# Kernel tuning notes

Measured on AMD Instinct MI355X. Metric: run time of the kernel, lower is better.

## Reference

```python
import jax, jax.numpy as jnp
import numpy as np

NUM_HEADS = 8
NUM_UNITS = 512


def setup_inputs() -> dict:
    key = jax.random.key(0)
    ks = jax.random.split(key, 5)
    B, S, D = 2, 4096, NUM_UNITS
    scale = 1.0 / np.sqrt(D)
    return {
        "x": jax.random.normal(ks[0], (B, S, D), dtype=jnp.float32),
        "Wq": jax.random.normal(ks[1], (D, NUM_UNITS), dtype=jnp.float32) * scale,
        "Wk": jax.random.normal(ks[2], (D, NUM_UNITS), dtype=jnp.float32) * scale,
        "Wv": jax.random.normal(ks[3], (D, NUM_UNITS), dtype=jnp.float32) * scale,
        "Wo": jax.random.normal(ks[4], (D, NUM_UNITS), dtype=jnp.float32) * scale,
    }


def reference(x, Wq, Wk, Wv, Wo):
    B, S, _ = x.shape
    H = NUM_HEADS
    Dh = NUM_UNITS // H

    # QKV linear projections (self-attention: K_V = (x, x))
    Q = x @ Wq  # [B,S,U]
    K = x @ Wk
    V = x @ Wv

    # split heads -> [B,H,S,Dh]
    def split(t):
        return t.reshape(B, S, H, Dh).transpose(0, 2, 1, 3)

    Qh, Kh, Vh = split(Q), split(K), split(V)

    # scaled dot-product attention, bias = 0, no mask, no dropout (training=False)
    scores = jnp.einsum("bhqd,bhkd->bhqk", Qh, Kh) / jnp.sqrt(
        jnp.asarray(Dh, dtype=x.dtype)
    )
    attn = jax.nn.softmax(scores, axis=-1)
    ctx = jnp.einsum("bhqk,bhkd->bhqd", attn, Vh)

    # combine heads -> [B,S,U], then output projection
    ctx = ctx.transpose(0, 2, 1, 3).reshape(B, S, NUM_UNITS)
    return ctx @ Wo
```

## Files before the change

### kernel.cpp

```cpp
#include <hip/hip_runtime.h>

typedef __attribute__((ext_vector_type(8))) short short8;
typedef __attribute__((ext_vector_type(4))) float f32x4;
typedef __attribute__((ext_vector_type(4))) unsigned short us4;
typedef unsigned short ushort_t;
typedef unsigned int uint_t;

typedef const __attribute__((address_space(1))) void* gas1;
typedef __attribute__((address_space(3))) void* las3;

#define LDS_FENCE()                                            \
  do {                                                         \
    asm volatile("s_waitcnt lgkmcnt(0)" ::: "memory");         \
    __builtin_amdgcn_sched_barrier(0);                         \
  } while (0)

__device__ __forceinline__ ushort_t f2b(float f) {
  union { float f; uint_t u; } v; v.f = f;
  return (ushort_t)((v.u + 0x7fffu + ((v.u >> 16) & 1u)) >> 16);
}

__device__ __forceinline__ float b2f(ushort_t u) {
  union { uint_t u; float f; } v; v.u = ((uint_t)u) << 16;
  return v.f;
}

__device__ __forceinline__ uint_t cvtpk(float lo, float hi) {
  uint_t r;
  asm("v_cvt_pk_bf16_f32 %0, %1, %2" : "=v"(r) : "v"(lo), "v"(hi));
  return r;
}

__device__ __forceinline__ void gld_lds16(const ushort_t* g, void* l) {
  __builtin_amdgcn_global_load_lds((gas1)g, (las3)l, 16, 0, 0);
}

__device__ __forceinline__ float max3f(float a, float b, float c) {
  return fmaxf(fmaxf(a, b), c);
}

__global__ void cvt_x_kernel(const float* __restrict__ x, ushort_t* __restrict__ xb, int n4) {
  int i = blockIdx.x * blockDim.x + threadIdx.x;
  if (i >= n4) return;
  float4 v = ((const float4*)x)[i];
  ushort4 o;
  o.x = f2b(v.x); o.y = f2b(v.y); o.z = f2b(v.z); o.w = f2b(v.w);
  ((ushort4*)xb)[i] = o;
}

__global__ void cvt_wt_kernel(const float* __restrict__ W0, const float* __restrict__ W1,
                              const float* __restrict__ W2, const float* __restrict__ W3,
                              ushort_t* __restrict__ T0, ushort_t* __restrict__ T1,
                              ushort_t* __restrict__ T2, ushort_t* __restrict__ T3) {
  const float* W; ushort_t* T;
  switch (blockIdx.z) {
    case 0: W = W0; T = T0; break;
    case 1: W = W1; T = T1; break;
    case 2: W = W2; T = T2; break;
    default: W = W3; T = T3; break;
  }
  __shared__ ushort_t Tl[64 * 68];
  int t = threadIdx.x;
  int kt = blockIdx.x & 7, nt = blockIdx.x >> 3;
  int krow = t >> 4;
  int ncol = (t & 15) * 4;
#pragma unroll
  for (int j = 0; j < 4; ++j) {
    int k = j * 16 + krow;
    float4 v = *(const float4*)&W[(size_t)(kt * 64 + k) * 512 + nt * 64 + ncol];
    const float* vf = (const float*)&v;
#pragma unroll
    for (int e = 0; e < 4; ++e)
      Tl[(ncol + e) * 68 + k] = f2b(vf[e]);
  }
  __syncthreads();
#pragma unroll
  for (int j = 0; j < 4; ++j) {
    int f = j * 1024 + t * 4;
    int n = f >> 6, k = f & 63;
    *(ushort4*)&T[(size_t)(nt * 64 + n) * 512 + kt * 64 + k] =
        *(const ushort4*)&Tl[n * 68 + k];
  }
}

__global__ __launch_bounds__(256) void gemm_qkv_kernel(
    const ushort_t* __restrict__ A,
    const ushort_t* __restrict__ WqT, const ushort_t* __restrict__ WkT,
    const ushort_t* __restrict__ WvT,
    ushort_t* __restrict__ Qo, ushort_t* __restrict__ Ko, ushort_t* __restrict__ VTo) {
  const int K = 512, N = 512, S = 4096;
  const ushort_t* BT; ushort_t* out; int mode;
  switch (blockIdx.z) {
    case 0: BT = WqT; out = Qo;  mode = 0; break;
    case 1: BT = WkT; out = Ko;  mode = 0; break;
    default: BT = WvT; out = VTo; mode = 1; break;
  }
  __shared__ ushort_t Al[128 * 64];
  __shared__ ushort_t Bl[128 * 64];

  int tid = threadIdx.x, lane = tid & 63, w = tid >> 6;
  int g = lane >> 4, ln = lane & 15;
  int wr = w >> 1, wc = w & 1;
  int m0 = blockIdx.y * 128;
  int n0 = blockIdx.x * 128;

  f32x4 acc[4][4];
  const f32x4 zz = {0.f, 0.f, 0.f, 0.f};
#pragma unroll
  for (int i = 0; i < 4; ++i)
#pragma unroll
    for (int j = 0; j < 4; ++j) acc[i][j] = zz;

  for (int kt = 0; kt < 8; ++kt) {
    __syncthreads();
#pragma unroll
    for (int i = 0; i < 4; ++i) {
      int p = i * 256 + tid, row = p >> 3, sl = p & 7, sp = sl ^ (row & 7);
      gld_lds16(A + (size_t)(m0 + row) * K + kt * 64 + sp * 8,
                (char*)Al + (i * 256 + (tid & 192)) * 16);
    }
#pragma unroll
    for (int i = 0; i < 4; ++i) {
      int p = i * 256 + tid, row = p >> 3, sl = p & 7, sp = sl ^ (row & 7);
      gld_lds16(BT + (size_t)(n0 + row) * K + kt * 64 + sp * 8,
                (char*)Bl + (i * 256 + (tid & 192)) * 16);
    }
    __syncthreads();

#pragma unroll
    for (int kc = 0; kc < 2; ++kc) {
      short8 af[4], bf[4];
#pragma unroll
      for (int mt = 0; mt < 4; ++mt) {
        int row = wr * 64 + mt * 16 + ln;
        af[mt] = *(const short8*)((char*)Al + row * 128 + (((kc * 4 + g) ^ (row & 7)) * 16));
      }
#pragma unroll
      for (int nt = 0; nt < 4; ++nt) {
        int row = wc * 64 + nt * 16 + ln;
        bf[nt] = *(const short8*)((char*)Bl + row * 128 + (((kc * 4 + g) ^ (row & 7)) * 16));
      }
#pragma unroll
      for (int mt = 0; mt < 4; ++mt)
#pragma unroll
        for (int nt = 0; nt < 4; ++nt)
          acc[mt][nt] = __builtin_amdgcn_mfma_f32_16x16x32_bf16(af[mt], bf[nt], acc[mt][nt], 0, 0, 0);
    }
  }

  if (mode == 0) {
#pragma unroll
    for (int mt = 0; mt < 4; ++mt)
#pragma unroll
      for (int nt = 0; nt < 4; ++nt)
#pragma unroll
        for (int jj = 0; jj < 4; ++jj) {
          int m = m0 + wr * 64 + mt * 16 + 4 * g + jj;
          int n = n0 + wc * 64 + nt * 16 + ln;
          out[(size_t)m * N + n] = f2b(acc[mt][nt][jj]);
        }
  } else {
#pragma unroll
    for (int mt = 0; mt < 4; ++mt)
#pragma unroll
      for (int nt = 0; nt < 4; ++nt) {
        int s0 = m0 + wr * 64 + mt * 16 + 4 * g;
        int u = n0 + wc * 64 + nt * 16 + ln;
        int b = s0 >> 12, s = s0 & 4095;
        int h = u >> 6, d = u & 63;
        us4 pv;
#pragma unroll
        for (int jj = 0; jj < 4; ++jj) pv[jj] = f2b(acc[mt][nt][jj]);
        *(us4*)&VTo[((size_t)((b * 8 + h) * 64 + d)) * S + s] = pv;
      }
  }
}

__global__ __launch_bounds__(256) void gemm_ao_kernel(
    const ushort_t* __restrict__ A, const ushort_t* __restrict__ BT,
    float* __restrict__ out) {
  const int K = 512, N = 512;
  __shared__ ushort_t Al[128 * 64];
  __shared__ ushort_t Bl[128 * 64];

  int tid = threadIdx.x, lane = tid & 63, w = tid >> 6;
  int g = lane >> 4, ln = lane & 15;
  int wr = w >> 1, wc = w & 1;
  int m0 = blockIdx.y * 128;
  int n0 = blockIdx.x * 128;

  f32x4 acc[4][4];
  const f32x4 zz = {0.f, 0.f, 0.f, 0.f};
#pragma unroll
  for (int i = 0; i < 4; ++i)
#pragma unroll
    for (int j = 0; j < 4; ++j) acc[i][j] = zz;

  for (int kt = 0; kt < 8; ++kt) {
    __syncthreads();
#pragma unroll
    for (int i = 0; i < 4; ++i) {
      int p = i * 256 + tid, row = p >> 3, sl = p & 7, sp = sl ^ (row & 7);
      gld_lds16(A + (size_t)(m0 + row) * K + kt * 64 + sp * 8,
                (char*)Al + (i * 256 + (tid & 192)) * 16);
    }
#pragma unroll
    for (int i = 0; i < 4; ++i) {
      int p = i * 256 + tid, row = p >> 3, sl = p & 7, sp = sl ^ (row & 7);
      gld_lds16(BT + (size_t)(n0 + row) * K + kt * 64 + sp * 8,
                (char*)Bl + (i * 256 + (tid & 192)) * 16);
    }
    __syncthreads();

#pragma unroll
    for (int kc = 0; kc < 2; ++kc) {
      short8 af[4], bf[4];
#pragma unroll
      for (int mt = 0; mt < 4; ++mt) {
        int row = wr * 64 + mt * 16 + ln;
        af[mt] = *(const short8*)((char*)Al + row * 128 + (((kc * 4 + g) ^ (row & 7)) * 16));
      }
#pragma unroll
      for (int nt = 0; nt < 4; ++nt) {
        int row = wc * 64 + nt * 16 + ln;
        bf[nt] = *(const short8*)((char*)Bl + row * 128 + (((kc * 4 + g) ^ (row & 7)) * 16));
      }
#pragma unroll
      for (int mt = 0; mt < 4; ++mt)
#pragma unroll
        for (int nt = 0; nt < 4; ++nt)
          acc[mt][nt] = __builtin_amdgcn_mfma_f32_16x16x32_bf16(af[mt], bf[nt], acc[mt][nt], 0, 0, 0);
    }
  }
#pragma unroll
  for (int mt = 0; mt < 4; ++mt)
#pragma unroll
    for (int nt = 0; nt < 4; ++nt)
#pragma unroll
      for (int jj = 0; jj < 4; ++jj) {
        int m = m0 + wr * 64 + mt * 16 + 4 * g + jj;
        int n = n0 + wc * 64 + nt * 16 + ln;
        out[(size_t)m * N + n] = acc[mt][nt][jj];
      }
}

__global__ __launch_bounds__(256) void attn_kernel(
    const ushort_t* __restrict__ Qg, const ushort_t* __restrict__ Kg,
    const ushort_t* __restrict__ VTg, ushort_t* __restrict__ Obuf,
    float* __restrict__ Lbuf, int ntiles) {
  const int S = 4096, U = 512, DH = 64;
  const float CSC = 0.125f * 1.44269504089f;
  int qb = blockIdx.x, h = blockIdx.y;
  int b = blockIdx.z & 1, part = blockIdx.z >> 1;
  int bh = b * 8 + h;
  int tid = threadIdx.x, lane = tid & 63, w = tid >> 6;
  int g = lane >> 4, ln = lane & 15;

  __shared__ ushort_t Kl[64 * 64];
  __shared__ ushort_t Vl[64 * 64];
  __shared__ ushort_t Pl[4][16 * 72];

  const ushort_t* qp = Qg + ((size_t)b * S + qb * 64 + w * 16 + ln) * U + h * DH + g * 8;
  short8 qf0 = *(const short8*)qp;
  short8 qf1 = *(const short8*)(qp + 32);

  f32x4 acc[4];
  const f32x4 zz = {0.f, 0.f, 0.f, 0.f};
#pragma unroll
  for (int i = 0; i < 4; ++i) acc[i] = zz;
  float mrun = -INFINITY, lrun = 0.f;

  int r = tid >> 3;
  int c8 = (tid & 7) * 8;
  const ushort_t* kbase = Kg + ((size_t)b * S + r) * U + h * DH + c8;
  const ushort_t* vbase = VTg + ((size_t)(bh * 64 + r)) * S + c8;

  int it0 = part * ntiles;
  for (int ii = 0; ii < ntiles; ++ii) {
    int kv0 = (it0 + ii) * 64;
    uint4 k1 = *(const uint4*)(kbase + (size_t)kv0 * U);
    uint4 k2 = *(const uint4*)(kbase + (size_t)(kv0 + 32) * U);
    uint4 v1 = *(const uint4*)(vbase + kv0);
    uint4 v2 = *(const uint4*)(vbase + (size_t)32 * S + kv0);
    __syncthreads();
    {
      int by1 = (r * 128 + c8 * 2) ^ ((r & 7) << 4);
      *(uint4*)((char*)Kl + by1) = k1;
      *(uint4*)((char*)Vl + by1) = v1;
      int r2 = r + 32;
      int by2 = (r2 * 128 + c8 * 2) ^ ((r2 & 7) << 4);
      *(uint4*)((char*)Kl + by2) = k2;
      *(uint4*)((char*)Vl + by2) = v2;
    }
    __syncthreads();

    f32x4 st[4];
#pragma unroll
    for (int m = 0; m < 4; ++m) {
      int row = m * 16 + ln;
      short8 kf0 = *(const short8*)((char*)Kl + ((row * 128 + 16 * g) ^ ((row & 7) << 4)));
      short8 kf1 = *(const short8*)((char*)Kl + ((row * 128 + 64 + 16 * g) ^ ((row & 7) << 4)));
      st[m] = __builtin_amdgcn_mfma_f32_16x16x32_bf16(kf0, qf0, zz, 0, 0, 0);
      st[m] = __builtin_amdgcn_mfma_f32_16x16x32_bf16(kf1, qf1, st[m], 0, 0, 0);
    }

    float t0 = max3f(st[0][0], st[0][1], st[0][2]);
    float t1 = max3f(st[0][3], st[1][0], st[1][1]);
    float t2 = max3f(st[1][2], st[1][3], st[2][0]);
    float t3 = max3f(st[2][1], st[2][2], st[2][3]);
    float t4 = max3f(st[3][0], st[3][1], st[3][2]);
    float smax = fmaxf(max3f(t0, t1, t2), max3f(t3, t4, st[3][3]));
    smax = fmaxf(smax, __shfl_xor(smax, 16));
    smax = fmaxf(smax, __shfl_xor(smax, 32));
    float tmax = smax * CSC;

    float mnew = fmaxf(mrun, tmax);
    if (!__all(tmax <= mrun + 8.0f)) {
      float alpha = __builtin_amdgcn_exp2f(mrun - mnew);
      mrun = mnew;
      lrun *= alpha;
      float av[4];
#pragma unroll
      for (int jj = 0; jj < 4; ++jj) av[jj] = __shfl(alpha, 4 * g + jj);
#pragma unroll
      for (int dt = 0; dt < 4; ++dt)
#pragma unroll
        for (int jj = 0; jj < 4; ++jj) acc[dt][jj] *= av[jj];
    }

    float nb = -mrun;
    float p[16];
    float ps = 0.f;
#pragma unroll
    for (int m = 0; m < 4; ++m)
#pragma unroll
      for (int jj = 0; jj < 4; ++jj) {
        float y = __builtin_amdgcn_exp2f(__builtin_fmaf(st[m][jj], CSC, nb));
        p[m * 4 + jj] = y;
        ps += y;
      }
    ps += __shfl_xor(ps, 16);
    ps += __shfl_xor(ps, 32);
    lrun += ps;

#pragma unroll
    for (int m = 0; m < 4; ++m) {
      uint2 pv;
      pv.x = cvtpk(p[m * 4 + 0], p[m * 4 + 1]);
      pv.y = cvtpk(p[m * 4 + 2], p[m * 4 + 3]);
      *(uint2*)&Pl[w][ln * 72 + m * 16 + 4 * g] = pv;
    }
    LDS_FENCE();

#pragma unroll
    for (int c = 0; c < 2; ++c) {
      short8 pf = *(const short8*)&Pl[w][ln * 72 + 32 * c + 8 * g];
#pragma unroll
      for (int dt = 0; dt < 4; ++dt) {
        int row = dt * 16 + ln;
        short8 vf = *(const short8*)((char*)Vl + ((row * 128 + 64 * c + 16 * g) ^ ((row & 7) << 4)));
        acc[dt] = __builtin_amdgcn_mfma_f32_16x16x32_bf16(pf, vf, acc[dt], 0, 0, 0);
      }
    }
  }

  float inv_l = 1.f / lrun;
  float lv[4];
#pragma unroll
  for (int jj = 0; jj < 4; ++jj) lv[jj] = __shfl(inv_l, 4 * g + jj);
  ushort_t* ob = Obuf + (size_t)part * 4194304 + ((size_t)bh * S) * 64;
#pragma unroll
  for (int dt = 0; dt < 4; ++dt)
#pragma unroll
    for (int jj = 0; jj < 4; ++jj) {
      int s = qb * 64 + w * 16 + 4 * g + jj;
      int d = dt * 16 + ln;
      ob[(size_t)s * 64 + d] = f2b(acc[dt][jj] * lv[jj]);
    }
  if (g == 0) {
    int s = qb * 64 + w * 16 + ln;
    Lbuf[part * 65536 + bh * S + s] = mrun + __log2f(lrun);
  }
}

__global__ void combine_kernel(const ushort_t* __restrict__ Obuf,
                               const float* __restrict__ Lbuf,
                               ushort_t* __restrict__ CTX, int nparts) {
  int tid = threadIdx.x;
  int row = blockIdx.x * 32 + (tid >> 3);
  int c = (tid & 7) * 8;
  int bh = row >> 12, s = row & 4095;
  int b = bh >> 3, h = bh & 7;

  us4 n0a = *(const us4*)&Obuf[(size_t)row * 64 + c];
  us4 n0b = *(const us4*)&Obuf[(size_t)row * 64 + c + 4];
  float o[8];
  if (nparts == 2) {
    float L0 = Lbuf[row];
    float L1 = Lbuf[65536 + row];
    us4 n1a = *(const us4*)&Obuf[(size_t)(4194304 + row * 64) + c];
    us4 n1b = *(const us4*)&Obuf[(size_t)(4194304 + row * 64) + c + 4];
    float Lm = fmaxf(L0, L1);
    float w0 = __builtin_amdgcn_exp2f(L0 - Lm);
    float w1 = __builtin_amdgcn_exp2f(L1 - Lm);
    float inv = 1.f / (w0 + w1);
    float a0 = w0 * inv, a1 = w1 * inv;
#pragma unroll
    for (int j = 0; j < 4; ++j) {
      o[j]     = a0 * b2f(n0a[j]) + a1 * b2f(n1a[j]);
      o[j + 4] = a0 * b2f(n0b[j]) + a1 * b2f(n1b[j]);
    }
  } else {
#pragma unroll
    for (int j = 0; j < 4; ++j) { o[j] = b2f(n0a[j]); o[j + 4] = b2f(n0b[j]); }
  }
  us4 w0v, w1v;
#pragma unroll
  for (int j = 0; j < 4; ++j) { w0v[j] = f2b(o[j]); w1v[j] = f2b(o[j + 4]); }
  ushort_t* dst = &CTX[((size_t)(b * 4096 + s)) * 512 + h * 64 + c];
  *(us4*)dst = w0v;
  *(us4*)(dst + 4) = w1v;
}

extern "C" void kernel_launch(void* const* d_in, const int* in_sizes, int n_in,
                              void* d_out, int out_size, void* d_ws, size_t ws_size,
                              hipStream_t stream) {
  const float* x  = (const float*)d_in[0];
  const float* Wq = (const float*)d_in[1];
  const float* Wk = (const float*)d_in[2];
  const float* Wv = (const float*)d_in[3];
  const float* Wo = (const float*)d_in[4];
  float* out = (float*)d_out;

  ushort_t* ws  = (ushort_t*)d_ws;
  ushort_t* xb  = ws;
  ushort_t* WqT = xb + 4194304;
  ushort_t* WkT = WqT + 262144;
  ushort_t* WvT = WkT + 262144;
  ushort_t* WoT = WvT + 262144;
  ushort_t* Qb  = WoT + 262144;
  ushort_t* Kb  = Qb + 4194304;
  ushort_t* VTb = Kb + 4194304;
  ushort_t* Obuf = VTb + 4194304;
  ushort_t* CTX = xb;

  int nparts = (ws_size >= 52953088u) ? 2 : 1;
  float* Lbuf = (float*)(Obuf + (size_t)nparts * 4194304);
  int ntiles = 64 / nparts;

  cvt_x_kernel<<<4096, 256, 0, stream>>>(x, xb, 1048576);
  cvt_wt_kernel<<<dim3(64, 1, 4), 256, 0, stream>>>(Wq, Wk, Wv, Wo, WqT, WkT, WvT, WoT);
  gemm_qkv_kernel<<<dim3(4, 64, 3), 256, 0, stream>>>(xb, WqT, WkT, WvT, Qb, Kb, VTb);
  attn_kernel<<<dim3(64, 8, 2 * nparts), 256, 0, stream>>>(Qb, Kb, VTb, Obuf, Lbuf, ntiles);
  combine_kernel<<<2048, 256, 0, stream>>>(Obuf, Lbuf, CTX, nparts);
  gemm_ao_kernel<<<dim3(4, 64), 256, 0, stream>>>(CTX, WoT, out);
}
```

Baseline: 249.4 us.

## Split attention KV tile across waves with cross-wave softmax and output reduction

The attention kernel now has each wave own 16 keys of the 64-key tile for all 64 queries, instead of owning 16 queries over all keys. P stays in registers and feeds 16x16x16 MFMAs directly, which removes the per-wave P round-trip through LDS. The price is two extra block barriers per tile to reduce row maxima across waves, plus a serialized four-pass accumulation of partial outputs through LDS at the end. Accumulator registers grow to 16 f32x4 per thread, which may lower occupancy.

```diff
diff --git a/kernel.cpp b/kernel.cpp
--- a/kernel.cpp
+++ b/kernel.cpp
@@ -1,6 +1,7 @@
 #include <hip/hip_runtime.h>
 
 typedef __attribute__((ext_vector_type(8))) short short8;
+typedef __attribute__((ext_vector_type(4))) short short4v;
 typedef __attribute__((ext_vector_type(4))) float f32x4;
 typedef __attribute__((ext_vector_type(4))) unsigned short us4;
 typedef unsigned short ushort_t;
@@ -9,12 +10,6 @@
 typedef const __attribute__((address_space(1))) void* gas1;
 typedef __attribute__((address_space(3))) void* las3;
 
-#define LDS_FENCE()                                            \
-  do {                                                         \
-    asm volatile("s_waitcnt lgkmcnt(0)" ::: "memory");         \
-    __builtin_amdgcn_sched_barrier(0);                         \
-  } while (0)
-
 __device__ __forceinline__ ushort_t f2b(float f) {
   union { float f; uint_t u; } v; v.f = f;
   return (ushort_t)((v.u + 0x7fffu + ((v.u >> 16) & 1u)) >> 16);
@@ -37,6 +32,17 @@
 
 __device__ __forceinline__ float max3f(float a, float b, float c) {
   return fmaxf(fmaxf(a, b), c);
+}
+
+__device__ __forceinline__ f32x4 mfma16(short4v a, short4v b, f32x4 c) {
+#if __has_builtin(__builtin_amdgcn_mfma_f32_16x16x16bf16_1k)
+  return __builtin_amdgcn_mfma_f32_16x16x16bf16_1k(a, b, c, 0, 0, 0);
+#else
+  f32x4 d = c;
+  asm volatile("v_mfma_f32_16x16x16_bf16 %0, %1, %2, %0\n\ts_nop 4"
+               : "+v"(d) : "v"(a), "v"(b));
+  return d;
+#endif
 }
 
 __global__ void cvt_x_kernel(const float* __restrict__ x, ushort_t* __restrict__ xb, int n4) {
@@ -248,7 +254,7 @@
     const ushort_t* __restrict__ Qg, const ushort_t* __restrict__ Kg,
     const ushort_t* __restrict__ VTg, ushort_t* __restrict__ Obuf,
     float* __restrict__ Lbuf, int ntiles) {
-  const int S = 4096, U = 512, DH = 64;
+  const int S = 4096, U = 512;
   const float CSC = 0.125f * 1.44269504089f;
   int qb = blockIdx.x, h = blockIdx.y;
   int b = blockIdx.z & 1, part = blockIdx.z >> 1;
@@ -256,23 +262,37 @@
   int tid = threadIdx.x, lane = tid & 63, w = tid >> 6;
   int g = lane >> 4, ln = lane & 15;
 
-  __shared__ ushort_t Kl[64 * 64];
-  __shared__ ushort_t Vl[64 * 64];
-  __shared__ ushort_t Pl[4][16 * 72];
-
-  const ushort_t* qp = Qg + ((size_t)b * S + qb * 64 + w * 16 + ln) * U + h * DH + g * 8;
-  short8 qf0 = *(const short8*)qp;
-  short8 qf1 = *(const short8*)(qp + 32);
-
-  f32x4 acc[4];
+  __shared__ __align__(16) char smem[17920];
+  ushort_t* Kl = (ushort_t*)smem;
+  ushort_t* Vl = (ushort_t*)(smem + 8192);
+  float* F    = (float*)smem;
+  float* wred = (float*)(smem + 16384);
+  float* Msh  = (float*)(smem + 17408);
+  float* Lsum = (float*)(smem + 17664);
+
+  short8 qf[4][2];
+  {
+    const ushort_t* qp0 = Qg + ((size_t)b * S + qb * 64 + ln) * U + h * 64 + g * 8;
+#pragma unroll
+    for (int n = 0; n < 4; ++n) {
+      qf[n][0] = *(const short8*)(qp0 + (size_t)(16 * n) * U);
+      qf[n][1] = *(const short8*)(qp0 + (size_t)(16 * n) * U + 32);
+    }
+  }
+
+  f32x4 acc[4][4];
   const f32x4 zz = {0.f, 0.f, 0.f, 0.f};
 #pragma unroll
-  for (int i = 0; i < 4; ++i) acc[i] = zz;
-  float mrun = -INFINITY, lrun = 0.f;
+  for (int i = 0; i < 4; ++i)
+#pragma unroll
+    for (int j = 0; j < 4; ++j) acc[i][j] = zz;
+  float mrun[4], lrun[4];
+#pragma unroll
+  for (int n = 0; n < 4; ++n) { mrun[n] = -INFINITY; lrun[n] = 0.f; }
 
   int r = tid >> 3;
   int c8 = (tid & 7) * 8;
-  const ushort_t* kbase = Kg + ((size_t)b * S + r) * U + h * DH + c8;
+  const ushort_t* kbase = Kg + ((size_t)b * S + r) * U + h * 64 + c8;
   const ushort_t* vbase = VTg + ((size_t)(bh * 64 + r)) * S + c8;
 
   int it0 = part * ntiles;
@@ -294,92 +314,133 @@
     }
     __syncthreads();
 
+    int arow = w * 16 + ln;
+    short8 kf0 = *(const short8*)((char*)Kl + ((arow * 128 + 16 * g) ^ ((arow & 7) << 4)));
+    short8 kf1 = *(const short8*)((char*)Kl + ((arow * 128 + 64 + 16 * g) ^ ((arow & 7) << 4)));
     f32x4 st[4];
 #pragma unroll
-    for (int m = 0; m < 4; ++m) {
-      int row = m * 16 + ln;
-      short8 kf0 = *(const short8*)((char*)Kl + ((row * 128 + 16 * g) ^ ((row & 7) << 4)));
-      short8 kf1 = *(const short8*)((char*)Kl + ((row * 128 + 64 + 16 * g) ^ ((row & 7) << 4)));
-      st[m] = __builtin_amdgcn_mfma_f32_16x16x32_bf16(kf0, qf0, zz, 0, 0, 0);
-      st[m] = __builtin_amdgcn_mfma_f32_16x16x32_bf16(kf1, qf1, st[m], 0, 0, 0);
-    }
-
-    float t0 = max3f(st[0][0], st[0][1], st[0][2]);
-    float t1 = max3f(st[0][3], st[1][0], st[1][1]);
-    float t2 = max3f(st[1][2], st[1][3], st[2][0]);
-    float t3 = max3f(st[2][1], st[2][2], st[2][3]);
-    float t4 = max3f(st[3][0], st[3][1], st[3][2]);
-    float smax = fmaxf(max3f(t0, t1, t2), max3f(t3, t4, st[3][3]));
-    smax = fmaxf(smax, __shfl_xor(smax, 16));
-    smax = fmaxf(smax, __shfl_xor(smax, 32));
-    float tmax = smax * CSC;
-
-    float mnew = fmaxf(mrun, tmax);
-    if (!__all(tmax <= mrun + 8.0f)) {
-      float alpha = __builtin_amdgcn_exp2f(mrun - mnew);
-      mrun = mnew;
-      lrun *= alpha;
-      float av[4];
-#pragma unroll
-      for (int jj = 0; jj < 4; ++jj) av[jj] = __shfl(alpha, 4 * g + jj);
+    for (int n = 0; n < 4; ++n) {
+      st[n] = __builtin_amdgcn_mfma_f32_16x16x32_bf16(kf0, qf[n][0], zz, 0, 0, 0);
+      st[n] = __builtin_amdgcn_mfma_f32_16x16x32_bf16(kf1, qf[n][1], st[n], 0, 0, 0);
+    }
+
+    float cmax[4];
+#pragma unroll
+    for (int n = 0; n < 4; ++n) {
+      float v = fmaxf(max3f(st[n][0], st[n][1], st[n][2]), st[n][3]);
+      v = fmaxf(v, __shfl_xor(v, 16));
+      v = fmaxf(v, __shfl_xor(v, 32));
+      cmax[n] = v;
+    }
+    if (g == 0) {
+#pragma unroll
+      for (int n = 0; n < 4; ++n) wred[w * 64 + 16 * n + ln] = cmax[n];
+    }
+    __syncthreads();
+    {
+      int q = tid >> 2;
+      float v = wred[(tid & 3) * 64 + q];
+      v = fmaxf(v, __shfl_xor(v, 1));
+      v = fmaxf(v, __shfl_xor(v, 2));
+      if ((tid & 3) == 0) Msh[q] = v;
+    }
+    __syncthreads();
+
+    float tm[4];
+#pragma unroll
+    for (int n = 0; n < 4; ++n) tm[n] = Msh[16 * n + ln] * CSC;
+    bool need = false;
+#pragma unroll
+    for (int n = 0; n < 4; ++n) need |= (tm[n] > mrun[n] + 8.0f);
+    if (__any(need)) {
+#pragma unroll
+      for (int n = 0; n < 4; ++n) {
+        float mn = fmaxf(mrun[n], tm[n]);
+        float al = __builtin_amdgcn_exp2f(mrun[n] - mn);
+        mrun[n] = mn;
+        lrun[n] *= al;
+#pragma unroll
+        for (int dt = 0; dt < 4; ++dt) acc[dt][n] *= al;
+      }
+    }
+
+    short4v pf[4];
+#pragma unroll
+    for (int n = 0; n < 4; ++n) {
+      float nb = -mrun[n];
+      float p0 = __builtin_amdgcn_exp2f(__builtin_fmaf(st[n][0], CSC, nb));
+      float p1 = __builtin_amdgcn_exp2f(__builtin_fmaf(st[n][1], CSC, nb));
+      float p2 = __builtin_amdgcn_exp2f(__builtin_fmaf(st[n][2], CSC, nb));
+      float p3 = __builtin_amdgcn_exp2f(__builtin_fmaf(st[n][3], CSC, nb));
+      union { uint_t u[2]; short4v s; } pu;
+      pu.u[0] = cvtpk(p0, p1);
+      pu.u[1] = cvtpk(p2, p3);
+      pf[n] = pu.s;
+      float ps = (p0 + p1) + (p2 + p3);
+      ps += __shfl_xor(ps, 16);
+      ps += __shfl_xor(ps, 32);
+      lrun[n] += ps;
+    }
+
+#pragma unroll
+    for (int dt = 0; dt < 4; ++dt) {
+      int vrow = dt * 16 + ln;
+      short4v vf = *(const short4v*)((char*)Vl +
+          ((vrow * 128 + 32 * w + 8 * g) ^ ((vrow & 7) << 4)));
+#pragma unroll
+      for (int n = 0; n < 4; ++n)
+        acc[dt][n] = mfma16(vf, pf[n], acc[dt][n]);
+    }
+  }
+
+  __syncthreads();
+  if (g == 0) {
+#pragma unroll
+    for (int n = 0; n < 4; ++n) {
+      wred[w * 64 + 16 * n + ln] = lrun[n];
+      if (w == 0) Msh[16 * n + ln] = mrun[n];
+    }
+  }
+  for (int rw = 0; rw < 4; ++rw) {
+    __syncthreads();
+    if (w == rw) {
 #pragma unroll
       for (int dt = 0; dt < 4; ++dt)
 #pragma unroll
-        for (int jj = 0; jj < 4; ++jj) acc[dt][jj] *= av[jj];
-    }
-
-    float nb = -mrun;
-    float p[16];
-    float ps = 0.f;
-#pragma unroll
-    for (int m = 0; m < 4; ++m)
-#pragma unroll
-      for (int jj = 0; jj < 4; ++jj) {
-        float y = __builtin_amdgcn_exp2f(__builtin_fmaf(st[m][jj], CSC, nb));
-        p[m * 4 + jj] = y;
-        ps += y;
-      }
-    ps += __shfl_xor(ps, 16);
-    ps += __shfl_xor(ps, 32);
-    lrun += ps;
-
-#pragma unroll
-    for (int m = 0; m < 4; ++m) {
-      uint2 pv;
-      pv.x = cvtpk(p[m * 4 + 0], p[m * 4 + 1]);
-      pv.y = cvtpk(p[m * 4 + 2], p[m * 4 + 3]);
-      *(uint2*)&Pl[w][ln * 72 + m * 16 + 4 * g] = pv;
-    }
-    LDS_FENCE();
-
-#pragma unroll
-    for (int c = 0; c < 2; ++c) {
-      short8 pf = *(const short8*)&Pl[w][ln * 72 + 32 * c + 8 * g];
-#pragma unroll
-      for (int dt = 0; dt < 4; ++dt) {
-        int row = dt * 16 + ln;
-        short8 vf = *(const short8*)((char*)Vl + ((row * 128 + 64 * c + 16 * g) ^ ((row & 7) << 4)));
-        acc[dt] = __builtin_amdgcn_mfma_f32_16x16x32_bf16(pf, vf, acc[dt], 0, 0, 0);
-      }
-    }
-  }
-
-  float inv_l = 1.f / lrun;
-  float lv[4];
-#pragma unroll
-  for (int jj = 0; jj < 4; ++jj) lv[jj] = __shfl(inv_l, 4 * g + jj);
-  ushort_t* ob = Obuf + (size_t)part * 4194304 + ((size_t)bh * S) * 64;
-#pragma unroll
-  for (int dt = 0; dt < 4; ++dt)
-#pragma unroll
-    for (int jj = 0; jj < 4; ++jj) {
-      int s = qb * 64 + w * 16 + 4 * g + jj;
-      int d = dt * 16 + ln;
-      ob[(size_t)s * 64 + d] = f2b(acc[dt][jj] * lv[jj]);
-    }
-  if (g == 0) {
-    int s = qb * 64 + w * 16 + ln;
-    Lbuf[part * 65536 + bh * S + s] = mrun + __log2f(lrun);
+        for (int n = 0; n < 4; ++n) {
+          int q = 16 * n + ln, d0 = dt * 16 + 4 * g;
+          char* fp = (char*)F + (((q * 64 + d0) * 4) ^ ((q & 7) << 4));
+          if (rw == 0) *(f32x4*)fp = acc[dt][n];
+          else         *(f32x4*)fp = acc[dt][n] + *(const f32x4*)fp;
+        }
+    }
+  }
+  __syncthreads();
+  {
+    int q = tid >> 2;
+    float v = wred[(tid & 3) * 64 + q];
+    v += __shfl_xor(v, 1);
+    v += __shfl_xor(v, 2);
+    if ((tid & 3) == 0) {
+      Lsum[q] = v;
+      Lbuf[part * 65536 + bh * S + qb * 64 + q] = Msh[q] + __log2f(v);
+    }
+  }
+  __syncthreads();
+  {
+    int q = tid >> 2, dg = (tid & 3) * 16;
+    float inv = 1.f / Lsum[q];
+    ushort_t* ob = Obuf + (size_t)part * 4194304 +
+                   ((size_t)bh * S + qb * 64 + q) * 64 + dg;
+#pragma unroll
+    for (int c = 0; c < 4; ++c) {
+      f32x4 vv = *(const f32x4*)((char*)F +
+          (((q * 64 + dg + 4 * c) * 4) ^ ((q & 7) << 4)));
+      us4 o;
+#pragma unroll
+      for (int j = 0; j < 4; ++j) o[j] = f2b(vv[j] * inv);
+      *(us4*)(ob + 4 * c) = o;
+    }
   }
 }
 
```

Result: slower. 345.8 us (+38.7%).

## Restructure attention kernel around 32x32 MFMA with register-resident P and prefetch

Applied to the files above, without the earlier changes.

The attention kernel moves from 16x16x32 to 32x32x16 bf16 MFMA tiles, with each of 8 waves handling 32 query rows, so a block covers 256 queries and the grid shrinks to match. The score layout is arranged so the probabilities can be packed straight into the A/B operand registers for the PV product. This removes the per-wave P staging through LDS and its fence, and cuts the row-max and row-sum shuffles to a single xor. Global loads for the next K/V tile are issued right after the barrier so they overlap with compute. The cost is higher register pressure under launch_bounds(512,4) and fewer blocks in flight.

```diff
diff --git a/kernel.cpp b/kernel.cpp
--- a/kernel.cpp
+++ b/kernel.cpp
@@ -2,18 +2,13 @@
 
 typedef __attribute__((ext_vector_type(8))) short short8;
 typedef __attribute__((ext_vector_type(4))) float f32x4;
+typedef __attribute__((ext_vector_type(16))) float f32x16;
 typedef __attribute__((ext_vector_type(4))) unsigned short us4;
 typedef unsigned short ushort_t;
 typedef unsigned int uint_t;
 
 typedef const __attribute__((address_space(1))) void* gas1;
 typedef __attribute__((address_space(3))) void* las3;
-
-#define LDS_FENCE()                                            \
-  do {                                                         \
-    asm volatile("s_waitcnt lgkmcnt(0)" ::: "memory");         \
-    __builtin_amdgcn_sched_barrier(0);                         \
-  } while (0)
 
 __device__ __forceinline__ ushort_t f2b(float f) {
   union { float f; uint_t u; } v; v.f = f;
@@ -37,6 +32,10 @@
 
 __device__ __forceinline__ float max3f(float a, float b, float c) {
   return fmaxf(fmaxf(a, b), c);
+}
+
+__device__ __forceinline__ f32x16 mfma32(short8 a, short8 b, f32x16 c) {
+  return __builtin_amdgcn_mfma_f32_32x32x16_bf16(a, b, c, 0, 0, 0);
 }
 
 __global__ void cvt_x_kernel(const float* __restrict__ x, ushort_t* __restrict__ xb, int n4) {
@@ -244,143 +243,156 @@
       }
 }
 
-__global__ __launch_bounds__(256) void attn_kernel(
+__global__ __launch_bounds__(512, 4) void attn_kernel(
     const ushort_t* __restrict__ Qg, const ushort_t* __restrict__ Kg,
     const ushort_t* __restrict__ VTg, ushort_t* __restrict__ Obuf,
     float* __restrict__ Lbuf, int ntiles) {
-  const int S = 4096, U = 512, DH = 64;
+  const int S = 4096, U = 512;
   const float CSC = 0.125f * 1.44269504089f;
   int qb = blockIdx.x, h = blockIdx.y;
   int b = blockIdx.z & 1, part = blockIdx.z >> 1;
   int bh = b * 8 + h;
   int tid = threadIdx.x, lane = tid & 63, w = tid >> 6;
-  int g = lane >> 4, ln = lane & 15;
+  int lq = lane & 31, hi = lane >> 5;
+  int lx = (lq & 7) << 4;
 
   __shared__ ushort_t Kl[64 * 64];
   __shared__ ushort_t Vl[64 * 64];
-  __shared__ ushort_t Pl[4][16 * 72];
-
-  const ushort_t* qp = Qg + ((size_t)b * S + qb * 64 + w * 16 + ln) * U + h * DH + g * 8;
-  short8 qf0 = *(const short8*)qp;
-  short8 qf1 = *(const short8*)(qp + 32);
-
-  f32x4 acc[4];
-  const f32x4 zz = {0.f, 0.f, 0.f, 0.f};
-#pragma unroll
-  for (int i = 0; i < 4; ++i) acc[i] = zz;
+
+  int qrow = qb * 256 + w * 32 + lq;
+  const ushort_t* qp = Qg + ((size_t)b * S + qrow) * U + h * 64 + hi * 8;
+  short8 qf[4];
+#pragma unroll
+  for (int s = 0; s < 4; ++s) qf[s] = *(const short8*)(qp + 16 * s);
+
+  f32x16 acc0 = {}, acc1 = {};
   float mrun = -INFINITY, lrun = 0.f;
 
-  int r = tid >> 3;
-  int c8 = (tid & 7) * 8;
-  const ushort_t* kbase = Kg + ((size_t)b * S + r) * U + h * DH + c8;
-  const ushort_t* vbase = VTg + ((size_t)(bh * 64 + r)) * S + c8;
-
+  int r = tid >> 3, c8 = (tid & 7) * 8;
+  int wby = (r * 128 + c8 * 2) ^ ((r & 7) << 4);
   int it0 = part * ntiles;
+  const ushort_t* kp = Kg + ((size_t)b * S + it0 * 64 + r) * U + h * 64 + c8;
+  const ushort_t* vp = VTg + ((size_t)(bh * 64 + r)) * S + it0 * 64 + c8;
+
+  uint4 kst = *(const uint4*)kp;
+  uint4 vst = *(const uint4*)vp;
+
+#define KREAD(rowv, colb) \
+  (*(const short8*)((char*)Kl + ((((rowv) * 128) + (colb)) ^ lx)))
+
+#define VREAD2(rowv, t, vout)                                             \
+  {                                                                       \
+    int base_ = (rowv) * 128 + 32 * (t) + 8 * hi;                         \
+    uint2 lo_ = *(const uint2*)((char*)Vl + (base_ ^ lx));                \
+    uint2 hi_ = *(const uint2*)((char*)Vl + ((base_ + 16) ^ lx));         \
+    union { uint_t u[4]; short8 s; } vu_;                                 \
+    vu_.u[0] = lo_.x; vu_.u[1] = lo_.y; vu_.u[2] = hi_.x; vu_.u[3] = hi_.y; \
+    vout = vu_.s;                                                         \
+  }
+
+#define MKPF(stv, ks, pfout)                                      \
+  {                                                               \
+    union { uint_t u[4]; short8 s; } pu;                          \
+    pu.u[0] = cvtpk(stv[8 * ks + 0], stv[8 * ks + 1]);            \
+    pu.u[1] = cvtpk(stv[8 * ks + 2], stv[8 * ks + 3]);            \
+    pu.u[2] = cvtpk(stv[8 * ks + 4], stv[8 * ks + 5]);            \
+    pu.u[3] = cvtpk(stv[8 * ks + 6], stv[8 * ks + 7]);            \
+    pfout = pu.s;                                                 \
+  }
+
   for (int ii = 0; ii < ntiles; ++ii) {
-    int kv0 = (it0 + ii) * 64;
-    uint4 k1 = *(const uint4*)(kbase + (size_t)kv0 * U);
-    uint4 k2 = *(const uint4*)(kbase + (size_t)(kv0 + 32) * U);
-    uint4 v1 = *(const uint4*)(vbase + kv0);
-    uint4 v2 = *(const uint4*)(vbase + (size_t)32 * S + kv0);
-    __syncthreads();
-    {
-      int by1 = (r * 128 + c8 * 2) ^ ((r & 7) << 4);
-      *(uint4*)((char*)Kl + by1) = k1;
-      *(uint4*)((char*)Vl + by1) = v1;
-      int r2 = r + 32;
-      int by2 = (r2 * 128 + c8 * 2) ^ ((r2 & 7) << 4);
-      *(uint4*)((char*)Kl + by2) = k2;
-      *(uint4*)((char*)Vl + by2) = v2;
-    }
-    __syncthreads();
-
-    f32x4 st[4];
-#pragma unroll
-    for (int m = 0; m < 4; ++m) {
-      int row = m * 16 + ln;
-      short8 kf0 = *(const short8*)((char*)Kl + ((row * 128 + 16 * g) ^ ((row & 7) << 4)));
-      short8 kf1 = *(const short8*)((char*)Kl + ((row * 128 + 64 + 16 * g) ^ ((row & 7) << 4)));
-      st[m] = __builtin_amdgcn_mfma_f32_16x16x32_bf16(kf0, qf0, zz, 0, 0, 0);
-      st[m] = __builtin_amdgcn_mfma_f32_16x16x32_bf16(kf1, qf1, st[m], 0, 0, 0);
-    }
-
-    float t0 = max3f(st[0][0], st[0][1], st[0][2]);
-    float t1 = max3f(st[0][3], st[1][0], st[1][1]);
-    float t2 = max3f(st[1][2], st[1][3], st[2][0]);
-    float t3 = max3f(st[2][1], st[2][2], st[2][3]);
-    float t4 = max3f(st[3][0], st[3][1], st[3][2]);
-    float smax = fmaxf(max3f(t0, t1, t2), max3f(t3, t4, st[3][3]));
-    smax = fmaxf(smax, __shfl_xor(smax, 16));
-    smax = fmaxf(smax, __shfl_xor(smax, 32));
-    float tmax = smax * CSC;
+    __syncthreads();
+    *(uint4*)((char*)Kl + wby) = kst;
+    *(uint4*)((char*)Vl + wby) = vst;
+    __syncthreads();
+    if (ii + 1 < ntiles) {
+      kp += (size_t)64 * U;
+      vp += 64;
+      kst = *(const uint4*)kp;
+      vst = *(const uint4*)vp;
+    }
+
+    f32x16 st0 = {}, st1 = {};
+#pragma unroll
+    for (int s = 0; s < 4; ++s)
+      st0 = mfma32(KREAD(lq, 32 * s + 16 * hi), qf[s], st0);
+#pragma unroll
+    for (int s = 0; s < 4; ++s)
+      st1 = mfma32(KREAD(32 + lq, 32 * s + 16 * hi), qf[s], st1);
+
+    float a0 = max3f(st0[0], st0[1], st0[2]);
+    float a1 = max3f(st0[3], st0[4], st0[5]);
+    float a2 = max3f(st0[6], st0[7], st0[8]);
+    float a3 = max3f(st0[9], st0[10], st0[11]);
+    float a4 = max3f(st0[12], st0[13], st0[14]);
+    float a5 = max3f(st0[15], st1[0], st1[1]);
+    float a6 = max3f(st1[2], st1[3], st1[4]);
+    float a7 = max3f(st1[5], st1[6], st1[7]);
+    float a8 = max3f(st1[8], st1[9], st1[10]);
+    float a9 = max3f(st1[11], st1[12], st1[13]);
+    float aa = fmaxf(st1[14], st1[15]);
+    float smax = fmaxf(fmaxf(max3f(a0, a1, a2), max3f(a3, a4, a5)),
+                       fmaxf(max3f(a6, a7, a8), fmaxf(a9, aa)));
+    float tmax = fmaxf(smax, __shfl_xor(smax, 32)) * CSC;
 
     float mnew = fmaxf(mrun, tmax);
     if (!__all(tmax <= mrun + 8.0f)) {
       float alpha = __builtin_amdgcn_exp2f(mrun - mnew);
       mrun = mnew;
       lrun *= alpha;
-      float av[4];
-#pragma unroll
-      for (int jj = 0; jj < 4; ++jj) av[jj] = __shfl(alpha, 4 * g + jj);
-#pragma unroll
-      for (int dt = 0; dt < 4; ++dt)
-#pragma unroll
-        for (int jj = 0; jj < 4; ++jj) acc[dt][jj] *= av[jj];
+#pragma unroll
+      for (int i = 0; i < 16; ++i) { acc0[i] *= alpha; acc1[i] *= alpha; }
     }
 
     float nb = -mrun;
-    float p[16];
     float ps = 0.f;
 #pragma unroll
-    for (int m = 0; m < 4; ++m)
-#pragma unroll
-      for (int jj = 0; jj < 4; ++jj) {
-        float y = __builtin_amdgcn_exp2f(__builtin_fmaf(st[m][jj], CSC, nb));
-        p[m * 4 + jj] = y;
-        ps += y;
-      }
-    ps += __shfl_xor(ps, 16);
+    for (int i = 0; i < 16; ++i) {
+      float y0 = __builtin_amdgcn_exp2f(__builtin_fmaf(st0[i], CSC, nb));
+      float y1 = __builtin_amdgcn_exp2f(__builtin_fmaf(st1[i], CSC, nb));
+      st0[i] = y0; st1[i] = y1;
+      ps += y0 + y1;
+    }
     ps += __shfl_xor(ps, 32);
     lrun += ps;
 
-#pragma unroll
-    for (int m = 0; m < 4; ++m) {
-      uint2 pv;
-      pv.x = cvtpk(p[m * 4 + 0], p[m * 4 + 1]);
-      pv.y = cvtpk(p[m * 4 + 2], p[m * 4 + 3]);
-      *(uint2*)&Pl[w][ln * 72 + m * 16 + 4 * g] = pv;
-    }
-    LDS_FENCE();
-
-#pragma unroll
-    for (int c = 0; c < 2; ++c) {
-      short8 pf = *(const short8*)&Pl[w][ln * 72 + 32 * c + 8 * g];
-#pragma unroll
-      for (int dt = 0; dt < 4; ++dt) {
-        int row = dt * 16 + ln;
-        short8 vf = *(const short8*)((char*)Vl + ((row * 128 + 64 * c + 16 * g) ^ ((row & 7) << 4)));
-        acc[dt] = __builtin_amdgcn_mfma_f32_16x16x32_bf16(pf, vf, acc[dt], 0, 0, 0);
-      }
-    }
-  }
-
-  float inv_l = 1.f / lrun;
-  float lv[4];
-#pragma unroll
-  for (int jj = 0; jj < 4; ++jj) lv[jj] = __shfl(inv_l, 4 * g + jj);
-  ushort_t* ob = Obuf + (size_t)part * 4194304 + ((size_t)bh * S) * 64;
-#pragma unroll
-  for (int dt = 0; dt < 4; ++dt)
-#pragma unroll
-    for (int jj = 0; jj < 4; ++jj) {
-      int s = qb * 64 + w * 16 + 4 * g + jj;
-      int d = dt * 16 + ln;
-      ob[(size_t)s * 64 + d] = f2b(acc[dt][jj] * lv[jj]);
-    }
-  if (g == 0) {
-    int s = qb * 64 + w * 16 + ln;
-    Lbuf[part * 65536 + bh * S + s] = mrun + __log2f(lrun);
-  }
+    short8 pf, vf;
+    MKPF(st0, 0, pf);
+    VREAD2(lq, 0, vf);      acc0 = mfma32(vf, pf, acc0);
+    VREAD2(32 + lq, 0, vf); acc1 = mfma32(vf, pf, acc1);
+    MKPF(st0, 1, pf);
+    VREAD2(lq, 1, vf);      acc0 = mfma32(vf, pf, acc0);
+    VREAD2(32 + lq, 1, vf); acc1 = mfma32(vf, pf, acc1);
+    MKPF(st1, 0, pf);
+    VREAD2(lq, 2, vf);      acc0 = mfma32(vf, pf, acc0);
+    VREAD2(32 + lq, 2, vf); acc1 = mfma32(vf, pf, acc1);
+    MKPF(st1, 1, pf);
+    VREAD2(lq, 3, vf);      acc0 = mfma32(vf, pf, acc0);
+    VREAD2(32 + lq, 3, vf); acc1 = mfma32(vf, pf, acc1);
+  }
+
+  float inv = 1.f / lrun;
+  ushort_t* ob = Obuf + (size_t)part * 4194304 +
+                 ((size_t)bh * S + qb * 256 + w * 32 + lq) * 64;
+#pragma unroll
+  for (int g4 = 0; g4 < 4; ++g4) {
+    uint2 o;
+    o.x = cvtpk(acc0[4 * g4 + 0] * inv, acc0[4 * g4 + 1] * inv);
+    o.y = cvtpk(acc0[4 * g4 + 2] * inv, acc0[4 * g4 + 3] * inv);
+    *(uint2*)(ob + 8 * g4 + 4 * hi) = o;
+  }
+#pragma unroll
+  for (int g4 = 0; g4 < 4; ++g4) {
+    uint2 o;
+    o.x = cvtpk(acc1[4 * g4 + 0] * inv, acc1[4 * g4 + 1] * inv);
+    o.y = cvtpk(acc1[4 * g4 + 2] * inv, acc1[4 * g4 + 3] * inv);
+    *(uint2*)(ob + 32 + 8 * g4 + 4 * hi) = o;
+  }
+  if (hi == 0)
+    Lbuf[part * 65536 + bh * S + qb * 256 + w * 32 + lq] = mrun + __log2f(lrun);
+#undef KREAD
+#undef VREAD2
+#undef MKPF
 }
 
 __global__ void combine_kernel(const ushort_t* __restrict__ Obuf,
@@ -451,7 +463,7 @@
   cvt_x_kernel<<<4096, 256, 0, stream>>>(x, xb, 1048576);
   cvt_wt_kernel<<<dim3(64, 1, 4), 256, 0, stream>>>(Wq, Wk, Wv, Wo, WqT, WkT, WvT, WoT);
   gemm_qkv_kernel<<<dim3(4, 64, 3), 256, 0, stream>>>(xb, WqT, WkT, WvT, Qb, Kb, VTb);
-  attn_kernel<<<dim3(64, 8, 2 * nparts), 256, 0, stream>>>(Qb, Kb, VTb, Obuf, Lbuf, ntiles);
+  attn_kernel<<<dim3(16, 8, 2 * nparts), 512, 0, stream>>>(Qb, Kb, VTb, Obuf, Lbuf, ntiles);
   combine_kernel<<<2048, 256, 0, stream>>>(Obuf, Lbuf, CTX, nparts);
   gemm_ao_kernel<<<dim3(4, 64), 256, 0, stream>>>(CTX, WoT, out);
 }
```

Measured after the change: 215.5 us. 13.6% less time.
